# Optimization experiments

Hardware: AMD Instinct MI355X
Metric: run time of the kernel (lower is better)

Reference implementation:

```python
import jax, jax.numpy as jnp
import numpy as np

B, N, IN_C, HID_C, OUT_C = 64, 1024, 16, 64, 32


def process_graph(graph):
    # graph: [B, N, N]; add self-loops, then row-normalize by inverse degree.
    n = graph.shape[-1]
    g = graph + jnp.eye(n, dtype=graph.dtype)
    deg = jnp.sum(g, axis=-1)                      # [B, N]
    inv_deg = jnp.where(deg == 0, jnp.zeros_like(deg), 1.0 / deg)
    # diag(inv_deg) @ g == row-wise broadcast scale (avoids O(N^3) diag matmul)
    return g * inv_deg[..., None]                  # [B, N, N]


def setup_inputs() -> dict:
    key = jax.random.key(0)
    kx, kg, k1, kb1, k2, kb2 = jax.random.split(key, 6)
    x = jax.random.normal(kx, (B, N, IN_C), dtype=jnp.float32)
    graph = jax.random.uniform(kg, (B, N, N), dtype=jnp.float32)
    # nn.Linear default init: U(-1/sqrt(fan_in), 1/sqrt(fan_in))
    lim1 = 1.0 / np.sqrt(IN_C)
    W1 = jax.random.uniform(k1, (HID_C, IN_C), minval=-lim1, maxval=lim1, dtype=jnp.float32)
    b1 = jax.random.uniform(kb1, (HID_C,), minval=-lim1, maxval=lim1, dtype=jnp.float32)
    lim2 = 1.0 / np.sqrt(HID_C)
    W2 = jax.random.uniform(k2, (OUT_C, HID_C), minval=-lim2, maxval=lim2, dtype=jnp.float32)
    b2 = jax.random.uniform(kb2, (OUT_C,), minval=-lim2, maxval=lim2, dtype=jnp.float32)
    return {"x": x, "graph": graph, "W1": W1, "b1": b1, "W2": W2, "b2": b2}


def reference(x, graph, W1, b1, W2, b2):
    g = process_graph(graph)                                   # [B, N, N]
    h = jnp.einsum('bnc,hc->bnh', x, W1) + b1                  # linear_1
    h = jax.nn.relu(jnp.einsum('bnm,bmh->bnh', g, h))          # propagate + ReLU
    o = jnp.einsum('bnh,oh->bno', h, W2) + b2                  # linear_2
    o = jax.nn.relu(jnp.einsum('bnm,bmo->bno', g, o))          # propagate + ReLU
    return o                                                   # [B, N, OUT_C]
```

## Files before the change

### kernel.cpp

```cpp
#include <hip/hip_runtime.h>

typedef __attribute__((ext_vector_type(8))) short s16x8;
typedef __attribute__((ext_vector_type(8))) unsigned short u16x8;
typedef __attribute__((ext_vector_type(4))) float f32x4;

#define B_   64
#define N_   1024
#define CIN_ 16
#define CH_  64
#define CO_  32

__device__ __forceinline__ unsigned short f2bf(float f){
  unsigned int u = __float_as_uint(f);
  u += 0x7fffu + ((u >> 16) & 1u);
  return (unsigned short)(u >> 16);
}

__global__ __launch_bounds__(256) void k_linear1(
    const float* __restrict__ x, const float* __restrict__ W1,
    const float* __restrict__ b1, unsigned short* __restrict__ H1T){
  int gt   = blockIdx.x * 256 + threadIdx.x;
  int wave = gt >> 6;
  int lane = gt & 63;
  int b    = wave >> 4;
  int nl0  = (wave & 15) << 6;

  const f32x4* xv = (const f32x4*)(x + ((size_t)(b * N_ + nl0 + lane)) * CIN_);
  float xr[16];
#pragma unroll
  for (int i = 0; i < 4; ++i){
    f32x4 v = xv[i];
#pragma unroll
    for (int e = 0; e < 4; ++e) xr[i*4+e] = v[e];
  }
  for (int h = 0; h < CH_; ++h){
    float acc = b1[h];
#pragma unroll
    for (int c = 0; c < CIN_; ++c) acc += xr[c] * W1[h * CIN_ + c];
    H1T[((size_t)(b * CH_ + h)) * N_ + nl0 + lane] = f2bf(acc);
  }
}

__global__ __launch_bounds__(256) void k_prop1(
    const float* __restrict__ graph, const unsigned short* __restrict__ H1T,
    const float* __restrict__ W2, const float* __restrict__ b2,
    unsigned short* __restrict__ O1T, unsigned short* __restrict__ GbT,
    float* __restrict__ idegw){
  __shared__ unsigned short sH2[4][16 * 64];

  const int b    = blockIdx.x >> 4;
  const int m0   = (blockIdx.x & 15) << 6;
  const int tid  = threadIdx.x;
  const int w    = tid >> 6, lane = tid & 63;
  const int l15  = lane & 15, lk = lane >> 4;
  const int gn   = m0 + (w << 4) + l15;
  const int ksd  = (m0 + (w << 4)) >> 5;

  const float* gA = graph + ((size_t)b << 20) + ((size_t)gn << 10) + (lk << 3);
  const unsigned short* hB = H1T + (size_t)(b * CH_ + l15) * N_ + (lk << 3);
  unsigned short* gW = GbT + ((size_t)b << 20) + ((size_t)gn << 10) + (lk << 3);

  f32x4 acc[4] = {{0,0,0,0},{0,0,0,0},{0,0,0,0},{0,0,0,0}};
  float deg = 0.f;

  f32x4 a0 = __builtin_nontemporal_load((const f32x4*)(gA));
  f32x4 a1 = __builtin_nontemporal_load((const f32x4*)(gA + 4));
  u16x8 b0 = *(const u16x8*)(hB);
  u16x8 b1f = *(const u16x8*)(hB + 16 * N_);
  u16x8 b2f = *(const u16x8*)(hB + 32 * N_);
  u16x8 b3f = *(const u16x8*)(hB + 48 * N_);

  for (int ks = 0; ks < 32; ++ks){
    const int kn = (((ks + 1) & 31) << 5);
    f32x4 na0 = __builtin_nontemporal_load((const f32x4*)(gA + kn));
    f32x4 na1 = __builtin_nontemporal_load((const f32x4*)(gA + kn + 4));
    u16x8 nb0 = *(const u16x8*)(hB + kn);
    u16x8 nb1 = *(const u16x8*)(hB + 16 * N_ + kn);
    u16x8 nb2 = *(const u16x8*)(hB + 32 * N_ + kn);
    u16x8 nb3 = *(const u16x8*)(hB + 48 * N_ + kn);

    float va[8] = {a0[0], a0[1], a0[2], a0[3], a1[0], a1[1], a1[2], a1[3]};
    if (ks == ksd){
      const int d0 = (ks << 5) + (lk << 3);
#pragma unroll
      for (int e = 0; e < 8; ++e) va[e] += (d0 + e == gn) ? 1.f : 0.f;
    }
#pragma unroll
    for (int e = 0; e < 8; ++e) deg += va[e];
    s16x8 af;
#pragma unroll
    for (int e = 0; e < 8; ++e) af[e] = (short)f2bf(va[e]);

    *(s16x8*)(gW + (ks << 5)) = af;

    acc[0] = __builtin_amdgcn_mfma_f32_16x16x32_bf16(af, (s16x8)b0,  acc[0], 0, 0, 0);
    acc[1] = __builtin_amdgcn_mfma_f32_16x16x32_bf16(af, (s16x8)b1f, acc[1], 0, 0, 0);
    acc[2] = __builtin_amdgcn_mfma_f32_16x16x32_bf16(af, (s16x8)b2f, acc[2], 0, 0, 0);
    acc[3] = __builtin_amdgcn_mfma_f32_16x16x32_bf16(af, (s16x8)b3f, acc[3], 0, 0, 0);

    a0 = na0; a1 = na1; b0 = nb0; b1f = nb1; b2f = nb2; b3f = nb3;
  }

  deg += __shfl_xor(deg, 16);
  deg += __shfl_xor(deg, 32);
  float ideg = 1.f / deg;
  if (lk == 0) idegw[(b << 10) + gn] = ideg;
  float idv[4];
#pragma unroll
  for (int j = 0; j < 4; ++j) idv[j] = __shfl(ideg, (lk << 2) + j);

#pragma unroll
  for (int cf = 0; cf < 4; ++cf){
#pragma unroll
    for (int j = 0; j < 4; ++j){
      float hv = acc[cf][j] * idv[j];
      hv = hv > 0.f ? hv : 0.f;
      int row = (lk << 2) + j;
      int col = (cf << 4) + l15;
      sH2[w][(row << 6) + (col ^ ((row & 7) << 3))] = f2bf(hv);
    }
  }
  __syncthreads();
  s16x8 a2[2];
#pragma unroll
  for (int kk = 0; kk < 2; ++kk)
    a2[kk] = *(const s16x8*)&sH2[w][(l15 << 6) + (((kk << 5) + (lk << 3)) ^ ((l15 & 7) << 3))];

  f32x4 acc2[2] = {{0,0,0,0},{0,0,0,0}};
#pragma unroll
  for (int kk = 0; kk < 2; ++kk){
#pragma unroll
    for (int cf = 0; cf < 2; ++cf){
      const f32x4* wp = (const f32x4*)(W2 + ((cf << 4) + l15) * CH_ + (kk << 5) + (lk << 3));
      f32x4 w0 = wp[0], w1 = wp[1];
      s16x8 bw;
#pragma unroll
      for (int e = 0; e < 4; ++e){ bw[e] = (short)f2bf(w0[e]); bw[4 + e] = (short)f2bf(w1[e]); }
      acc2[cf] = __builtin_amdgcn_mfma_f32_16x16x32_bf16(a2[kk], bw, acc2[cf], 0, 0, 0);
    }
  }
#pragma unroll
  for (int cf = 0; cf < 2; ++cf){
    float badd = b2[(cf << 4) + l15];
#pragma unroll
    for (int j = 0; j < 4; ++j){
      float v = acc2[cf][j] + badd;
      int n = m0 + (w << 4) + (lk << 2) + j;
      O1T[((size_t)(b * CO_ + (cf << 4) + l15)) * N_ + n] = f2bf(v);
    }
  }
}

__global__ __launch_bounds__(256) void k_prop2(
    const unsigned short* __restrict__ GbT, const unsigned short* __restrict__ O1T,
    const float* __restrict__ idegw, float* __restrict__ out){
  const int b    = blockIdx.x >> 4;
  const int m0   = (blockIdx.x & 15) << 6;
  const int tid  = threadIdx.x;
  const int w    = tid >> 6, lane = tid & 63;
  const int l15  = lane & 15, lk = lane >> 4;
  const int gn   = m0 + (w << 4) + l15;

  const unsigned short* gA = GbT + ((size_t)b << 20) + ((size_t)gn << 10) + (lk << 3);
  const unsigned short* oB = O1T + (size_t)(b * CO_ + l15) * N_ + (lk << 3);

  f32x4 acc[2] = {{0,0,0,0},{0,0,0,0}};

  u16x8 aP0 = *(const u16x8*)(gA + (31 << 5));
  u16x8 bP0 = *(const u16x8*)(oB + (31 << 5));
  u16x8 cP0 = *(const u16x8*)(oB + 16 * N_ + (31 << 5));
  u16x8 aP1 = *(const u16x8*)(gA + (30 << 5));
  u16x8 bP1 = *(const u16x8*)(oB + (30 << 5));
  u16x8 cP1 = *(const u16x8*)(oB + 16 * N_ + (30 << 5));

#pragma unroll 4
  for (int ks = 31; ks >= 0; --ks){
    const int kn = ((ks + 30) & 31) << 5;
    u16x8 na = *(const u16x8*)(gA + kn);
    u16x8 nb = *(const u16x8*)(oB + kn);
    u16x8 nc = *(const u16x8*)(oB + 16 * N_ + kn);

    acc[0] = __builtin_amdgcn_mfma_f32_16x16x32_bf16((s16x8)aP0, (s16x8)bP0, acc[0], 0, 0, 0);
    acc[1] = __builtin_amdgcn_mfma_f32_16x16x32_bf16((s16x8)aP0, (s16x8)cP0, acc[1], 0, 0, 0);

    aP0 = aP1; bP0 = bP1; cP0 = cP1;
    aP1 = na;  bP1 = nb;  cP1 = nc;
  }

  f32x4 idv = *(const f32x4*)(idegw + (b << 10) + m0 + (w << 4) + (lk << 2));

#pragma unroll
  for (int cf = 0; cf < 2; ++cf){
#pragma unroll
    for (int j = 0; j < 4; ++j){
      float v = acc[cf][j] * idv[j];
      v = v > 0.f ? v : 0.f;
      int n = m0 + (w << 4) + (lk << 2) + j;
      out[((size_t)(b * N_ + n)) * CO_ + (cf << 4) + l15] = v;
    }
  }
}

extern "C" void kernel_launch(void* const* d_in, const int* in_sizes, int n_in,
                              void* d_out, int out_size, void* d_ws, size_t ws_size,
                              hipStream_t stream){
  (void)in_sizes; (void)n_in; (void)out_size; (void)ws_size;
  const float* x     = (const float*)d_in[0];
  const float* graph = (const float*)d_in[1];
  const float* W1    = (const float*)d_in[2];
  const float* b1    = (const float*)d_in[3];
  const float* W2    = (const float*)d_in[4];
  const float* b2    = (const float*)d_in[5];
  float* out = (float*)d_out;

  unsigned short* H1T = (unsigned short*)d_ws;
  unsigned short* O1T = (unsigned short*)((char*)d_ws + ((size_t)8 << 20));
  float*        idegw = (float*)((char*)d_ws + ((size_t)12 << 20));
  unsigned short* GbT = (unsigned short*)((char*)d_ws + ((size_t)16 << 20));

  k_linear1<<<256, 256, 0, stream>>>(x, W1, b1, H1T);
  k_prop1<<<B_ * 16, 256, 0, stream>>>(graph, H1T, W2, b2, O1T, GbT, idegw);
  k_prop2<<<B_ * 16, 256, 0, stream>>>(GbT, O1T, idegw, out);
}
```

Measured before the change: 507.3 us.

## Split graph conversion into a separate tiled-layout kernel and use LDS double-buffered GEMMs

Adds a streaming conversion kernel that reads the fp32 graph once, adds self-loops, computes partial degrees and writes bf16 into a tile-contiguous, XOR-swizzled layout. A small kernel then reduces the partials to inverse degrees. Both propagation kernels now stage contiguous 64x64 tiles of the graph and features into double-buffered shared memory, instead of doing strided per-lane global loads. The aim is better coalescing and memory throughput, at the cost of two extra launches and an extra write and read of the bf16 graph in the prop1 path.

Result: faster. 473.8 us (-6.6%).

```diff
diff --git a/kernel.cpp b/kernel.cpp
--- a/kernel.cpp
+++ b/kernel.cpp
@@ -2,6 +2,7 @@
 
 typedef __attribute__((ext_vector_type(8))) short s16x8;
 typedef __attribute__((ext_vector_type(8))) unsigned short u16x8;
+typedef __attribute__((ext_vector_type(4))) unsigned short u16x4;
 typedef __attribute__((ext_vector_type(4))) float f32x4;
 
 #define B_   64
@@ -20,8 +21,7 @@
     const float* __restrict__ x, const float* __restrict__ W1,
     const float* __restrict__ b1, unsigned short* __restrict__ H1T){
   int gt   = blockIdx.x * 256 + threadIdx.x;
-  int wave = gt >> 6;
-  int lane = gt & 63;
+  int wave = gt >> 6, lane = gt & 63;
   int b    = wave >> 4;
   int nl0  = (wave & 15) << 6;
 
@@ -41,74 +41,112 @@
   }
 }
 
+__global__ __launch_bounds__(256) void k_convert(
+    const float* __restrict__ graph, unsigned short* __restrict__ GbT,
+    float* __restrict__ degp){
+  const int t    = blockIdx.x * 256 + threadIdx.x;
+  const int lane = threadIdx.x & 63;
+
+  size_t i  = (size_t)t;
+  f32x4 v   = *(const f32x4*)(graph + (i << 2));
+  for (int it = 0; it < 32; ++it){
+    size_t inext = (size_t)t + (size_t)((it + 1) & 31) * 524288;
+    f32x4 vn = *(const f32x4*)(graph + (inext << 2));
+
+    const size_t fbase   = i << 2;
+    const int rowflat    = (int)(fbase >> 10);
+    const int row_in_b   = rowflat & 1023;
+    const int c0         = (int)(fbase & 1023);
+    const int d          = row_in_b - c0;
+    if (d >= 0 && d < 4) v[d] += 1.f;
+
+    float s = v[0] + v[1] + v[2] + v[3];
+    s += __shfl_xor(s, 1);  s += __shfl_xor(s, 2);  s += __shfl_xor(s, 4);
+    s += __shfl_xor(s, 8);  s += __shfl_xor(s, 16); s += __shfl_xor(s, 32);
+    if (lane == 0) degp[(size_t)rowflat * 4 + ((c0 >> 8) & 3)] = s;
+
+    const int b     = rowflat >> 10;
+    const int mtile = row_in_b >> 6, srow = row_in_b & 63;
+    const int ks    = c0 >> 6,       colt = c0 & 63;
+    const int c8s   = (colt >> 3) ^ (srow & 7);
+    const size_t dst = ((((size_t)(b * 16 + mtile) * 16 + ks) * 64 + srow) * 8 + c8s) * 8
+                       + (colt & 7);
+    u16x4 o;
+#pragma unroll
+    for (int e = 0; e < 4; ++e) o[e] = f2bf(v[e]);
+    *(u16x4*)(GbT + dst) = o;
+
+    i = inext; v = vn;
+  }
+}
+
+__global__ __launch_bounds__(256) void k_ideg(
+    const float* __restrict__ degp, float* __restrict__ idegw){
+  int i = blockIdx.x * 256 + threadIdx.x;
+  f32x4 d = *(const f32x4*)(degp + (size_t)i * 4);
+  idegw[i] = 1.f / (d[0] + d[1] + d[2] + d[3]);
+}
+
 __global__ __launch_bounds__(256) void k_prop1(
-    const float* __restrict__ graph, const unsigned short* __restrict__ H1T,
+    const unsigned short* __restrict__ GbT, const unsigned short* __restrict__ H1T,
     const float* __restrict__ W2, const float* __restrict__ b2,
-    unsigned short* __restrict__ O1T, unsigned short* __restrict__ GbT,
-    float* __restrict__ idegw){
-  __shared__ unsigned short sH2[4][16 * 64];
-
-  const int b    = blockIdx.x >> 4;
-  const int m0   = (blockIdx.x & 15) << 6;
-  const int tid  = threadIdx.x;
-  const int w    = tid >> 6, lane = tid & 63;
-  const int l15  = lane & 15, lk = lane >> 4;
-  const int gn   = m0 + (w << 4) + l15;
-  const int ksd  = (m0 + (w << 4)) >> 5;
-
-  const float* gA = graph + ((size_t)b << 20) + ((size_t)gn << 10) + (lk << 3);
-  const unsigned short* hB = H1T + (size_t)(b * CH_ + l15) * N_ + (lk << 3);
-  unsigned short* gW = GbT + ((size_t)b << 20) + ((size_t)gn << 10) + (lk << 3);
+    const float* __restrict__ idegw, unsigned short* __restrict__ O1T){
+  __shared__ unsigned short sA[2][4096];
+  __shared__ unsigned short sB[2][4096];
+  __shared__ unsigned short sH2[4][1024];
+
+  const int b = blockIdx.x >> 4, mtile = blockIdx.x & 15, m0 = mtile << 6;
+  const int tid = threadIdx.x, w = tid >> 6, lane = tid & 63;
+  const int l15 = lane & 15, lk = lane >> 4;
+
+  const unsigned short* gA = GbT + ((size_t)(b * 16 + mtile) << 16);
+  const unsigned short* hB = H1T + ((size_t)b << 16);
+
+  const int ch0 = tid, ch1 = 256 + tid;
+  const int r0 = ch0 >> 3, r1 = ch1 >> 3;
+  const size_t bs0 = (size_t)r0 * N_ + (((ch0 & 7) ^ (r0 & 7)) << 3);
+  const size_t bs1 = (size_t)r1 * N_ + (((ch1 & 7) ^ (r1 & 7)) << 3);
 
   f32x4 acc[4] = {{0,0,0,0},{0,0,0,0},{0,0,0,0},{0,0,0,0}};
-  float deg = 0.f;
-
-  f32x4 a0 = __builtin_nontemporal_load((const f32x4*)(gA));
-  f32x4 a1 = __builtin_nontemporal_load((const f32x4*)(gA + 4));
-  u16x8 b0 = *(const u16x8*)(hB);
-  u16x8 b1f = *(const u16x8*)(hB + 16 * N_);
-  u16x8 b2f = *(const u16x8*)(hB + 32 * N_);
-  u16x8 b3f = *(const u16x8*)(hB + 48 * N_);
-
-  for (int ks = 0; ks < 32; ++ks){
-    const int kn = (((ks + 1) & 31) << 5);
-    f32x4 na0 = __builtin_nontemporal_load((const f32x4*)(gA + kn));
-    f32x4 na1 = __builtin_nontemporal_load((const f32x4*)(gA + kn + 4));
-    u16x8 nb0 = *(const u16x8*)(hB + kn);
-    u16x8 nb1 = *(const u16x8*)(hB + 16 * N_ + kn);
-    u16x8 nb2 = *(const u16x8*)(hB + 32 * N_ + kn);
-    u16x8 nb3 = *(const u16x8*)(hB + 48 * N_ + kn);
-
-    float va[8] = {a0[0], a0[1], a0[2], a0[3], a1[0], a1[1], a1[2], a1[3]};
-    if (ks == ksd){
-      const int d0 = (ks << 5) + (lk << 3);
-#pragma unroll
-      for (int e = 0; e < 8; ++e) va[e] += (d0 + e == gn) ? 1.f : 0.f;
-    }
-#pragma unroll
-    for (int e = 0; e < 8; ++e) deg += va[e];
-    s16x8 af;
-#pragma unroll
-    for (int e = 0; e < 8; ++e) af[e] = (short)f2bf(va[e]);
-
-    *(s16x8*)(gW + (ks << 5)) = af;
-
-    acc[0] = __builtin_amdgcn_mfma_f32_16x16x32_bf16(af, (s16x8)b0,  acc[0], 0, 0, 0);
-    acc[1] = __builtin_amdgcn_mfma_f32_16x16x32_bf16(af, (s16x8)b1f, acc[1], 0, 0, 0);
-    acc[2] = __builtin_amdgcn_mfma_f32_16x16x32_bf16(af, (s16x8)b2f, acc[2], 0, 0, 0);
-    acc[3] = __builtin_amdgcn_mfma_f32_16x16x32_bf16(af, (s16x8)b3f, acc[3], 0, 0, 0);
-
-    a0 = na0; a1 = na1; b0 = nb0; b1f = nb1; b2f = nb2; b3f = nb3;
-  }
-
-  deg += __shfl_xor(deg, 16);
-  deg += __shfl_xor(deg, 32);
-  float ideg = 1.f / deg;
-  if (lk == 0) idegw[(b << 10) + gn] = ideg;
-  float idv[4];
-#pragma unroll
-  for (int j = 0; j < 4; ++j) idv[j] = __shfl(ideg, (lk << 2) + j);
-
+
+  {
+    u16x8 a0 = *(const u16x8*)(gA + ch0 * 8);
+    u16x8 a1 = *(const u16x8*)(gA + ch1 * 8);
+    u16x8 h0 = *(const u16x8*)(hB + bs0);
+    u16x8 h1 = *(const u16x8*)(hB + bs1);
+    *(u16x8*)&sA[0][ch0 * 8] = a0;  *(u16x8*)&sA[0][ch1 * 8] = a1;
+    *(u16x8*)&sB[0][ch0 * 8] = h0;  *(u16x8*)&sB[0][ch1 * 8] = h1;
+  }
+  __syncthreads();
+
+  int buf = 0;
+  const int arow = (w << 4) + l15;
+  for (int ks = 0; ks < 16; ++ks){
+    const int kn = (ks + 1) & 15;
+    u16x8 na0 = *(const u16x8*)(gA + (size_t)kn * 4096 + ch0 * 8);
+    u16x8 na1 = *(const u16x8*)(gA + (size_t)kn * 4096 + ch1 * 8);
+    u16x8 nh0 = *(const u16x8*)(hB + bs0 + kn * 64);
+    u16x8 nh1 = *(const u16x8*)(hB + bs1 + kn * 64);
+
+#pragma unroll
+    for (int kk = 0; kk < 2; ++kk){
+      s16x8 a = *(const s16x8*)&sA[buf][arow * 64 + ((((kk << 2) + lk) ^ (arow & 7)) << 3)];
+#pragma unroll
+      for (int cf = 0; cf < 4; ++cf){
+        const int brow = (cf << 4) + l15;
+        s16x8 bb = *(const s16x8*)&sB[buf][brow * 64 + ((((kk << 2) + lk) ^ (brow & 7)) << 3)];
+        acc[cf] = __builtin_amdgcn_mfma_f32_16x16x32_bf16(a, bb, acc[cf], 0, 0, 0);
+      }
+    }
+    if (ks < 15){
+      *(u16x8*)&sA[buf ^ 1][ch0 * 8] = na0;  *(u16x8*)&sA[buf ^ 1][ch1 * 8] = na1;
+      *(u16x8*)&sB[buf ^ 1][ch0 * 8] = nh0;  *(u16x8*)&sB[buf ^ 1][ch1 * 8] = nh1;
+    }
+    __syncthreads();
+    buf ^= 1;
+  }
+
+  f32x4 idv = *(const f32x4*)(idegw + (b << 10) + m0 + (w << 4) + (lk << 2));
 #pragma unroll
   for (int cf = 0; cf < 4; ++cf){
 #pragma unroll
@@ -154,41 +192,58 @@
 __global__ __launch_bounds__(256) void k_prop2(
     const unsigned short* __restrict__ GbT, const unsigned short* __restrict__ O1T,
     const float* __restrict__ idegw, float* __restrict__ out){
-  const int b    = blockIdx.x >> 4;
-  const int m0   = (blockIdx.x & 15) << 6;
-  const int tid  = threadIdx.x;
-  const int w    = tid >> 6, lane = tid & 63;
-  const int l15  = lane & 15, lk = lane >> 4;
-  const int gn   = m0 + (w << 4) + l15;
-
-  const unsigned short* gA = GbT + ((size_t)b << 20) + ((size_t)gn << 10) + (lk << 3);
-  const unsigned short* oB = O1T + (size_t)(b * CO_ + l15) * N_ + (lk << 3);
+  __shared__ unsigned short sA[2][4096];
+  __shared__ unsigned short sB[2][2048];
+
+  const int b = blockIdx.x >> 4, mtile = blockIdx.x & 15, m0 = mtile << 6;
+  const int tid = threadIdx.x, w = tid >> 6, lane = tid & 63;
+  const int l15 = lane & 15, lk = lane >> 4;
+
+  const unsigned short* gA = GbT + ((size_t)(b * 16 + mtile) << 16);
+  const unsigned short* oB = O1T + ((size_t)b << 15);
+
+  const int ch0 = tid, ch1 = 256 + tid;
+  const int rB = tid >> 3;
+  const size_t bs = (size_t)rB * N_ + (((tid & 7) ^ (rB & 7)) << 3);
 
   f32x4 acc[2] = {{0,0,0,0},{0,0,0,0}};
 
-  u16x8 aP0 = *(const u16x8*)(gA + (31 << 5));
-  u16x8 bP0 = *(const u16x8*)(oB + (31 << 5));
-  u16x8 cP0 = *(const u16x8*)(oB + 16 * N_ + (31 << 5));
-  u16x8 aP1 = *(const u16x8*)(gA + (30 << 5));
-  u16x8 bP1 = *(const u16x8*)(oB + (30 << 5));
-  u16x8 cP1 = *(const u16x8*)(oB + 16 * N_ + (30 << 5));
-
-#pragma unroll 4
-  for (int ks = 31; ks >= 0; --ks){
-    const int kn = ((ks + 30) & 31) << 5;
-    u16x8 na = *(const u16x8*)(gA + kn);
-    u16x8 nb = *(const u16x8*)(oB + kn);
-    u16x8 nc = *(const u16x8*)(oB + 16 * N_ + kn);
-
-    acc[0] = __builtin_amdgcn_mfma_f32_16x16x32_bf16((s16x8)aP0, (s16x8)bP0, acc[0], 0, 0, 0);
-    acc[1] = __builtin_amdgcn_mfma_f32_16x16x32_bf16((s16x8)aP0, (s16x8)cP0, acc[1], 0, 0, 0);
-
-    aP0 = aP1; bP0 = bP1; cP0 = cP1;
-    aP1 = na;  bP1 = nb;  cP1 = nc;
+  {
+    u16x8 a0 = *(const u16x8*)(gA + ch0 * 8);
+    u16x8 a1 = *(const u16x8*)(gA + ch1 * 8);
+    u16x8 o0 = *(const u16x8*)(oB + bs);
+    *(u16x8*)&sA[0][ch0 * 8] = a0;  *(u16x8*)&sA[0][ch1 * 8] = a1;
+    *(u16x8*)&sB[0][tid * 8] = o0;
+  }
+  __syncthreads();
+
+  int buf = 0;
+  const int arow = (w << 4) + l15;
+  for (int ks = 0; ks < 16; ++ks){
+    const int kn = (ks + 1) & 15;
+    u16x8 na0 = *(const u16x8*)(gA + (size_t)kn * 4096 + ch0 * 8);
+    u16x8 na1 = *(const u16x8*)(gA + (size_t)kn * 4096 + ch1 * 8);
+    u16x8 no0 = *(const u16x8*)(oB + bs + kn * 64);
+
+#pragma unroll
+    for (int kk = 0; kk < 2; ++kk){
+      s16x8 a = *(const s16x8*)&sA[buf][arow * 64 + ((((kk << 2) + lk) ^ (arow & 7)) << 3)];
+#pragma unroll
+      for (int cf = 0; cf < 2; ++cf){
+        const int brow = (cf << 4) + l15;
+        s16x8 bb = *(const s16x8*)&sB[buf][brow * 64 + ((((kk << 2) + lk) ^ (brow & 7)) << 3)];
+        acc[cf] = __builtin_amdgcn_mfma_f32_16x16x32_bf16(a, bb, acc[cf], 0, 0, 0);
+      }
+    }
+    if (ks < 15){
+      *(u16x8*)&sA[buf ^ 1][ch0 * 8] = na0;  *(u16x8*)&sA[buf ^ 1][ch1 * 8] = na1;
+      *(u16x8*)&sB[buf ^ 1][tid * 8] = no0;
+    }
+    __syncthreads();
+    buf ^= 1;
   }
 
   f32x4 idv = *(const f32x4*)(idegw + (b << 10) + m0 + (w << 4) + (lk << 2));
-
 #pragma unroll
   for (int cf = 0; cf < 2; ++cf){
 #pragma unroll
@@ -216,9 +271,12 @@
   unsigned short* H1T = (unsigned short*)d_ws;
   unsigned short* O1T = (unsigned short*)((char*)d_ws + ((size_t)8 << 20));
   float*        idegw = (float*)((char*)d_ws + ((size_t)12 << 20));
+  float*         degp = (float*)((char*)d_ws + ((size_t)13 << 20));
   unsigned short* GbT = (unsigned short*)((char*)d_ws + ((size_t)16 << 20));
 
-  k_linear1<<<256, 256, 0, stream>>>(x, W1, b1, H1T);
-  k_prop1<<<B_ * 16, 256, 0, stream>>>(graph, H1T, W2, b2, O1T, GbT, idegw);
-  k_prop2<<<B_ * 16, 256, 0, stream>>>(GbT, O1T, idegw, out);
-}
+  k_linear1<<<256,  256, 0, stream>>>(x, W1, b1, H1T);
+  k_convert<<<2048, 256, 0, stream>>>(graph, GbT, degp);
+  k_ideg   <<<256,  256, 0, stream>>>(degp, idegw);
+  k_prop1  <<<B_ * 16, 256, 0, stream>>>(GbT, H1T, W2, b2, idegw, O1T);
+  k_prop2  <<<B_ * 16, 256, 0, stream>>>(GbT, O1T, idegw, out);
+}
```
